# Kernel optimization log

Measured on AMD Instinct MI355X. Metric: run time of the kernel, lower is better.

Reference implementation:

```python
import jax, jax.numpy as jnp
import numpy as np

SH_DIM = 9                      # (sh_deg+1)^2, sh_deg=2
DATA_DIM = SH_DIM * 3 + 1       # 28
FINE = 8
COARSE = 32
RADIUS = 1.3
NUM_ATOMS = 16
BATCH = 128
STEP = (RADIUS * 2.0 / COARSE / FINE) / 2.0   # fine_voxel_len / 2
N_INTRS = COARSE * 3 * 2 * FINE               # 1536


def sh_encode(dirs):
    # degree-2 real spherical harmonics bases, [.., 9]
    x, y, z = dirs[..., 0], dirs[..., 1], dirs[..., 2]
    C0 = 0.28209479177387814
    C1 = 0.4886025119029199
    C2 = (1.0925484305920792, -1.0925484305920792, 0.31539156525252005,
          -1.0925484305920792, 0.5462742152960396)
    return jnp.stack([
        jnp.full_like(x, C0), -C1 * y, C1 * z, -C1 * x,
        C2[0] * x * y, C2[1] * y * z, C2[2] * (2.0 * z * z - x * x - y * y),
        C2[3] * x * z, C2[4] * (x * x - y * y)], axis=-1)


def dict_interp(grid, atoms, pts):
    # pts: [N,3] normalized to [0,1). grid: [COARSE^3, A]. atoms: [FINE^3, A, D].
    # coarse voxel -> dictionary coefficients; trilinear interp of atoms inside it.
    cpos = pts * COARSE
    cidx = jnp.clip(jnp.floor(cpos), 0, COARSE - 1)
    ci = cidx.astype(jnp.int32)
    coeff = grid[(ci[:, 0] * COARSE + ci[:, 1]) * COARSE + ci[:, 2]]  # [N, A]
    local = cpos - cidx                       # [0,1) within coarse voxel
    fpos = local * FINE - 0.5
    f0f = jnp.floor(fpos)
    w = fpos - f0f                            # trilinear weights
    f0 = f0f.astype(jnp.int32)
    out = jnp.zeros((pts.shape[0], DATA_DIM), dtype=pts.dtype)
    for dx in (0, 1):
        for dy in (0, 1):
            for dz in (0, 1):
                ix = jnp.clip(f0[:, 0] + dx, 0, FINE - 1)
                iy = jnp.clip(f0[:, 1] + dy, 0, FINE - 1)
                iz = jnp.clip(f0[:, 2] + dz, 0, FINE - 1)
                wt = ((w[:, 0] if dx else 1.0 - w[:, 0]) *
                      (w[:, 1] if dy else 1.0 - w[:, 1]) *
                      (w[:, 2] if dz else 1.0 - w[:, 2]))
                vals = jnp.einsum('na,nad->nd', coeff, atoms[(ix * FINE + iy) * FINE + iz])
                out = out + wt[:, None] * vals
    return out


def setup_inputs() -> dict:
    key = jax.random.key(0)
    k1, k2, k3, k4 = jax.random.split(key, 4)
    rays_o = jnp.array([0.0, 0.0, -2.0 * RADIUS]) + 0.05 * jax.random.normal(k1, (BATCH, 3), jnp.float32)
    d = 0.25 * jax.random.normal(k2, (BATCH, 3), jnp.float32) + jnp.array([0.0, 0.0, 1.0])
    rays_d = d / jnp.linalg.norm(d, axis=-1, keepdims=True)
    grid = 0.01 * jax.random.normal(k3, (COARSE ** 3, NUM_ATOMS), jnp.float32)
    atoms_sh = jax.random.uniform(k4, (FINE ** 3, NUM_ATOMS, DATA_DIM - 1), jnp.float32)
    atoms = jnp.concatenate([atoms_sh, jnp.full((FINE ** 3, NUM_ATOMS, 1), 0.01, jnp.float32)], -1)
    return {"rays_o": rays_o, "rays_d": rays_d, "grid": grid, "atoms": atoms, "grid_id": 0}


def reference(rays_o, rays_d, grid, atoms, grid_id):
    B = rays_o.shape[0]
    # ---- sample_proposal (no-grad in original) ----
    off_pos = (RADIUS - rays_o) / rays_d
    off_neg = (-RADIUS - rays_o) / rays_d
    start = jnp.max(jnp.minimum(off_pos, off_neg), axis=-1, keepdims=True)
    steps = jnp.arange(N_INTRS, dtype=rays_o.dtype)[None, :]
    intersections = jax.lax.stop_gradient(start + steps * STEP)        # [B, 1536]
    tsec = intersections[:, :-1]                                       # [B, M]
    M = N_INTRS - 1
    pts = rays_o[:, None, :] + tsec[:, :, None] * rays_d[:, None, :]   # [B, M, 3]
    mask = jnp.all((pts > -RADIUS) & (pts < RADIUS), axis=-1)          # [B, M]
    pts_n = jnp.clip((pts + RADIUS) / (2.0 * RADIUS), 0.0, 1.0 - 1e-6)
    pts_n = jax.lax.stop_gradient(pts_n).reshape(-1, 3)
    # ---- dictionary interpolation (computed densely, zeroed by mask) ----
    data = dict_interp(grid, atoms, pts_n).reshape(B, M, DATA_DIM)
    sigma = jax.nn.relu(jnp.where(mask, data[..., -1], 0.0))           # [B, M]
    # ---- sigma -> alpha / weights ----
    dists = (intersections[:, 1:] - intersections[:, :-1]) * jnp.linalg.norm(rays_d, axis=-1, keepdims=True)
    alpha = 1.0 - jnp.exp(-sigma * dists)
    trans = jnp.concatenate([jnp.ones((B, 1), alpha.dtype),
                             jnp.cumprod(1.0 - alpha + 1e-10, axis=-1)[:, :-1]], axis=-1)
    abs_light = alpha * trans                                          # [B, M]
    # ---- SH -> rgb, composite ----
    sh_mult = sh_encode(rays_d)[:, None, None, :]                      # [B,1,1,9]
    sh = data[..., :-1].reshape(B, M, 3, SH_DIM)
    rgb_raw = jnp.where(mask[..., None], jnp.sum(sh_mult * sh, axis=-1), 0.0)  # [B,M,3]
    rgb = jnp.sum(abs_light[..., None] * jax.nn.sigmoid(rgb_raw), axis=1)
    rgb = rgb + (1.0 - jnp.sum(abs_light, axis=-1))[:, None]           # white background
    depth = jnp.sum(abs_light * tsec, axis=-1)
    return rgb, alpha, depth
```

## Files before the change

kernel.cpp:

```cpp
#include <hip/hip_runtime.h>

typedef unsigned int u32;

#define MSAMP 1535
#define NS 1024
#define RADF 1.3f
#define STEPF ((float)(1.3 * 2.0 / 32.0 / 8.0 / 2.0))
#define NCELLG 32768
#define CSCALE 0.06f
#define PRANGE 4.0f

#if __has_builtin(__builtin_amdgcn_sdot4)
#define SDOT4(a, b, c) __builtin_amdgcn_sdot4((a), (b), (c), false)
#else
static __device__ __forceinline__ int SDOT4(int a, int b, int c) {
#pragma unroll
    for (int i = 0; i < 4; i++) {
        int ai = (a << (24 - 8 * i)) >> 24;
        int bi = (b << (24 - 8 * i)) >> 24;
        c += ai * bi;
    }
    return c;
}
#endif

__device__ __forceinline__ u32 q4(float a, float b, float c, float d, float S) {
    int i0 = (int)rintf(fminf(fmaxf(a * S, -127.0f), 127.0f));
    int i1 = (int)rintf(fminf(fmaxf(b * S, -127.0f), 127.0f));
    int i2 = (int)rintf(fminf(fmaxf(c * S, -127.0f), 127.0f));
    int i3 = (int)rintf(fminf(fmaxf(d * S, -127.0f), 127.0f));
    return (u32)(i0 & 255) | ((u32)(i1 & 255) << 8) | ((u32)(i2 & 255) << 16)
         | ((u32)(i3 & 255) << 24);
}

__global__ __launch_bounds__(256) void k_prep(const float* __restrict__ rd,
                                              const float* __restrict__ atoms,
                                              const float* __restrict__ grid,
                                              uint4* __restrict__ Pq,
                                              uint4* __restrict__ gridq) {
    __shared__ __align__(16) float af[448];
    int b = blockIdx.x, t = threadIdx.x;
    if (b < 512) {
        if (t < 112) ((float4*)af)[t] = ((const float4*)(atoms + b * 448))[t];
        int r = t & 127;
        float dx = rd[r * 3 + 0], dy = rd[r * 3 + 1], dz = rd[r * 3 + 2];
        float shm[9];
        shm[0] = 0.28209479177387814f;
        shm[1] = -0.4886025119029199f * dy;
        shm[2] =  0.4886025119029199f * dz;
        shm[3] = -0.4886025119029199f * dx;
        shm[4] =  1.0925484305920792f * dx * dy;
        shm[5] = -1.0925484305920792f * dy * dz;
        shm[6] =  0.31539156525252005f * (2.0f * dz * dz - dx * dx - dy * dy);
        shm[7] = -1.0925484305920792f * dx * dz;
        shm[8] =  0.5462742152960396f * (dx * dx - dy * dy);
        __syncthreads();
#pragma unroll
        for (int iter = 0; iter < 2; iter++) {
            int ch = (t >> 7) + 2 * iter;
            u32 w[4] = {0u, 0u, 0u, 0u};
            if (ch < 3) {
                const float S = 127.0f / PRANGE;
#pragma unroll
                for (int a = 0; a < 16; a++) {
                    const float* ap = af + a * 28 + ch * 9;
                    float p = shm[0] * ap[0];
#pragma unroll
                    for (int k = 1; k < 9; k++) p = fmaf(shm[k], ap[k], p);
                    int q = (int)rintf(fminf(fmaxf(p * S, -127.0f), 127.0f));
                    w[a >> 2] |= ((u32)(q & 255)) << (8 * (a & 3));
                }
            } else {
#pragma unroll
                for (int a = 0; a < 16; a++) {
                    float p = af[a * 28 + 27];
                    int q = (int)rintf(fminf(fmaxf(p * 127.0f, -127.0f), 127.0f));
                    w[a >> 2] |= ((u32)(q & 255)) << (8 * (a & 3));
                }
            }
            Pq[b * 512 + r * 4 + ch] = make_uint4(w[0], w[1], w[2], w[3]);
        }
    } else {
        int cell = (b - 512) * 256 + t;
        const float4* gp = (const float4*)(grid + cell * 16);
        float4 c0 = gp[0], c1 = gp[1], c2 = gp[2], c3 = gp[3];
        const float S = 127.0f / CSCALE;
        uint4 outv;
        outv.x = q4(c0.x, c0.y, c0.z, c0.w, S);
        outv.y = q4(c1.x, c1.y, c1.z, c1.w, S);
        outv.z = q4(c2.x, c2.y, c2.z, c2.w, S);
        outv.w = q4(c3.x, c3.y, c3.z, c3.w, S);
        gridq[cell] = outv;
    }
}

__global__ __launch_bounds__(1024) void k_main(const float* __restrict__ ro,
                                               const float* __restrict__ rd,
                                               const uint4* __restrict__ gridq,
                                               const uint4* __restrict__ Pq,
                                               float* __restrict__ rgb_out,
                                               float* __restrict__ alpha_out,
                                               float* __restrict__ depth_out) {
    __shared__ __align__(16) signed char hl[512 * 80];
    __shared__ float wprod[16];
    __shared__ float wred[16][5];
    int ray = blockIdx.x;
    int t = threadIdx.x;
    int lane = t & 63, wave = t >> 6;

#pragma unroll
    for (int i = 0; i < 2; i++) {
        int idx = i * 1024 + t;
        int cell = idx >> 2, part = idx & 3;
        uint4 v = Pq[cell * 512 + ray * 4 + part];
        *(uint4*)&hl[cell * 80 + part * 16] = v;
    }

    int abase = ray * MSAMP;
    if (NS + t < MSAMP) alpha_out[abase + NS + t] = 0.0f;

    float ox = ro[ray * 3 + 0], oy = ro[ray * 3 + 1], oz = ro[ray * 3 + 2];
    float dx = rd[ray * 3 + 0], dy = rd[ray * 3 + 1], dz = rd[ray * 3 + 2];
    float a0 = ( RADF - ox) / dx, b0 = (-RADF - ox) / dx;
    float a1 = ( RADF - oy) / dy, b1 = (-RADF - oy) / dy;
    float a2 = ( RADF - oz) / dz, b2 = (-RADF - oz) / dz;
    float st = fmaxf(fmaxf(fminf(a0, b0), fminf(a1, b1)), fminf(a2, b2));
    float nrm = sqrtf(dx * dx + dy * dy + dz * dz);

    __syncthreads();

    float tm = st + (float)t * STEPF;
    float px = ox + tm * dx, py = oy + tm * dy, pz = oz + tm * dz;
    bool inb = (px > -RADF) && (px < RADF) && (py > -RADF) && (py < RADF)
            && (pz > -RADF) && (pz < RADF);

    float acc[4] = {0.0f, 0.0f, 0.0f, 0.0f};
    if (inb) {
        const float inv2R = 1.0f / 2.6f;
        float pnx = fminf(fmaxf((px + RADF) * inv2R, 0.0f), 0.999999f);
        float pny = fminf(fmaxf((py + RADF) * inv2R, 0.0f), 0.999999f);
        float pnz = fminf(fmaxf((pz + RADF) * inv2R, 0.0f), 0.999999f);

        float cpx = pnx * 32.0f, cpy = pny * 32.0f, cpz = pnz * 32.0f;
        float cfx = floorf(cpx), cfy = floorf(cpy), cfz = floorf(cpz);
        int cix = (int)cfx, ciy = (int)cfy, ciz = (int)cfz;

        float fpx = (cpx - cfx) * 8.0f - 0.5f;
        float fpy = (cpy - cfy) * 8.0f - 0.5f;
        float fpz = (cpz - cfz) * 8.0f - 0.5f;
        float ffx = floorf(fpx), ffy = floorf(fpy), ffz = floorf(fpz);
        int f0x = (int)ffx, f0y = (int)ffy, f0z = (int)ffz;
        float wx = fpx - ffx, wy = fpy - ffy, wz = fpz - ffz;

        int ixa[2] = { max(f0x, 0), min(f0x + 1, 7) };
        int iya[2] = { max(f0y, 0), min(f0y + 1, 7) };
        int iza[2] = { max(f0z, 0), min(f0z + 1, 7) };
        float wxa[2] = { 1.0f - wx, wx };
        float wya[2] = { 1.0f - wy, wy };
        float wza[2] = { 1.0f - wz, wz };

        uint4 cq = gridq[(cix * 32 + ciy) * 32 + ciz];

#pragma unroll
        for (int cx = 0; cx < 2; cx++)
#pragma unroll
        for (int cy = 0; cy < 2; cy++)
#pragma unroll
        for (int cz = 0; cz < 2; cz++) {
            float wt = wxa[cx] * wya[cy] * wza[cz];
            int cb = ((ixa[cx] * 8 + iya[cy]) * 8 + iza[cz]) * 80;
#pragma unroll
            for (int j = 0; j < 4; j++) {
                uint4 qa = *(const uint4*)&hl[cb + j * 16];
                int di = SDOT4((int)qa.x, (int)cq.x, 0);
                di = SDOT4((int)qa.y, (int)cq.y, di);
                di = SDOT4((int)qa.z, (int)cq.z, di);
                di = SDOT4((int)qa.w, (int)cq.w, di);
                acc[j] = fmaf(wt, (float)di, acc[j]);
            }
        }
    }

    const float QSC = CSCALE / (127.0f * 127.0f);
    const float RSC = QSC * PRANGE;
    float sigma = fmaxf(acc[3] * QSC, 0.0f);
    float alpha = 1.0f - __expf(-sigma * STEPF * nrm);
    float r0 = 1.0f / (1.0f + __expf(-acc[0] * RSC));
    float r1 = 1.0f / (1.0f + __expf(-acc[1] * RSC));
    float r2 = 1.0f / (1.0f + __expf(-acc[2] * RSC));
    alpha_out[abase + t] = alpha;

    float p = 1.0f - alpha + 1e-10f;
    float incl = p;
#pragma unroll
    for (int off = 1; off < 64; off <<= 1) {
        float vv = __shfl_up(incl, off);
        if (lane >= off) incl *= vv;
    }
    if (lane == 63) wprod[wave] = incl;
    __syncthreads();
    float excl = __shfl_up(incl, 1);
    if (lane == 0) excl = 1.0f;
    for (int w = 0; w < 16; w++) if (w < wave) excl *= wprod[w];

    float w_ = alpha * excl;
    float vals[5] = { w_ * r0, w_ * r1, w_ * r2, w_ * tm, w_ };
#pragma unroll
    for (int i = 0; i < 5; i++) {
        float v = vals[i];
        v += __shfl_xor(v, 1);  v += __shfl_xor(v, 2);  v += __shfl_xor(v, 4);
        v += __shfl_xor(v, 8);  v += __shfl_xor(v, 16); v += __shfl_xor(v, 32);
        if (lane == 0) wred[wave][i] = v;
    }
    __syncthreads();
    if (t == 0) {
        float res[5];
#pragma unroll
        for (int i = 0; i < 5; i++) {
            float r_ = 0.0f;
            for (int w = 0; w < 16; w++) r_ += wred[w][i];
            res[i] = r_;
        }
        float omw = 1.0f - res[4];
        rgb_out[ray * 3 + 0] = res[0] + omw;
        rgb_out[ray * 3 + 1] = res[1] + omw;
        rgb_out[ray * 3 + 2] = res[2] + omw;
        depth_out[ray] = res[3];
    }
}

extern "C" void kernel_launch(void* const* d_in, const int* in_sizes, int n_in,
                              void* d_out, int out_size, void* d_ws, size_t ws_size,
                              hipStream_t stream) {
    const float* ro    = (const float*)d_in[0];
    const float* rd    = (const float*)d_in[1];
    const float* grid  = (const float*)d_in[2];
    const float* atoms = (const float*)d_in[3];
    int B = in_sizes[0] / 3;

    uint4* gridq = (uint4*)d_ws;
    uint4* Pq    = (uint4*)((char*)d_ws + 524288);

    float* out       = (float*)d_out;
    float* rgb_out   = out;
    float* alpha_out = out + B * 3;
    float* depth_out = out + B * 3 + B * MSAMP;

    hipLaunchKernelGGL(k_prep, dim3(640), dim3(256), 0, stream,
                       rd, atoms, grid, Pq, gridq);
    hipLaunchKernelGGL(k_main, dim3(B), dim3(1024), 0, stream,
                       ro, rd, (const uint4*)gridq, (const uint4*)Pq,
                       rgb_out, alpha_out, depth_out);
}
```

Before: 74.84 us.

## Shrink LDS atom stride to 72 bytes, transpose atoms in prep, issue global loads early

```diff
diff --git a/kernel.cpp b/kernel.cpp
--- a/kernel.cpp
+++ b/kernel.cpp
@@ -9,6 +9,7 @@
 #define NCELLG 32768
 #define CSCALE 0.06f
 #define PRANGE 4.0f
+#define HSTRIDE 72
 
 #if __has_builtin(__builtin_amdgcn_sdot4)
 #define SDOT4(a, b, c) __builtin_amdgcn_sdot4((a), (b), (c), false)
@@ -38,10 +39,19 @@
                                               const float* __restrict__ grid,
                                               uint4* __restrict__ Pq,
                                               uint4* __restrict__ gridq) {
-    __shared__ __align__(16) float af[448];
+    __shared__ __align__(16) float af2[28 * 16];
     int b = blockIdx.x, t = threadIdx.x;
     if (b < 512) {
-        if (t < 112) ((float4*)af)[t] = ((const float4*)(atoms + b * 448))[t];
+        if (t < 112) {
+            float4 v = ((const float4*)(atoms + b * 448))[t];
+            int i0 = t * 4;
+#pragma unroll
+            for (int u = 0; u < 4; u++) {
+                int i = i0 + u;
+                int a = i / 28, d = i - a * 28;
+                af2[d * 16 + a] = (&v.x)[u];
+            }
+        }
         int r = t & 127;
         float dx = rd[r * 3 + 0], dy = rd[r * 3 + 1], dz = rd[r * 3 + 2];
         float shm[9];
@@ -58,25 +68,45 @@
 #pragma unroll
         for (int iter = 0; iter < 2; iter++) {
             int ch = (t >> 7) + 2 * iter;
-            u32 w[4] = {0u, 0u, 0u, 0u};
+            float p[16];
+            float S;
             if (ch < 3) {
-                const float S = 127.0f / PRANGE;
-#pragma unroll
-                for (int a = 0; a < 16; a++) {
-                    const float* ap = af + a * 28 + ch * 9;
-                    float p = shm[0] * ap[0];
-#pragma unroll
-                    for (int k = 1; k < 9; k++) p = fmaf(shm[k], ap[k], p);
-                    int q = (int)rintf(fminf(fmaxf(p * S, -127.0f), 127.0f));
-                    w[a >> 2] |= ((u32)(q & 255)) << (8 * (a & 3));
+                S = 127.0f / PRANGE;
+#pragma unroll
+                for (int k = 0; k < 9; k++) {
+                    const float4* row = (const float4*)&af2[(ch * 9 + k) * 16];
+                    float4 q0 = row[0], q1 = row[1], q2 = row[2], q3 = row[3];
+                    float s = shm[k];
+                    if (k == 0) {
+                        p[0]=s*q0.x;  p[1]=s*q0.y;  p[2]=s*q0.z;  p[3]=s*q0.w;
+                        p[4]=s*q1.x;  p[5]=s*q1.y;  p[6]=s*q1.z;  p[7]=s*q1.w;
+                        p[8]=s*q2.x;  p[9]=s*q2.y;  p[10]=s*q2.z; p[11]=s*q2.w;
+                        p[12]=s*q3.x; p[13]=s*q3.y; p[14]=s*q3.z; p[15]=s*q3.w;
+                    } else {
+                        p[0]=fmaf(s,q0.x,p[0]);   p[1]=fmaf(s,q0.y,p[1]);
+                        p[2]=fmaf(s,q0.z,p[2]);   p[3]=fmaf(s,q0.w,p[3]);
+                        p[4]=fmaf(s,q1.x,p[4]);   p[5]=fmaf(s,q1.y,p[5]);
+                        p[6]=fmaf(s,q1.z,p[6]);   p[7]=fmaf(s,q1.w,p[7]);
+                        p[8]=fmaf(s,q2.x,p[8]);   p[9]=fmaf(s,q2.y,p[9]);
+                        p[10]=fmaf(s,q2.z,p[10]); p[11]=fmaf(s,q2.w,p[11]);
+                        p[12]=fmaf(s,q3.x,p[12]); p[13]=fmaf(s,q3.y,p[13]);
+                        p[14]=fmaf(s,q3.z,p[14]); p[15]=fmaf(s,q3.w,p[15]);
+                    }
                 }
             } else {
-#pragma unroll
-                for (int a = 0; a < 16; a++) {
-                    float p = af[a * 28 + 27];
-                    int q = (int)rintf(fminf(fmaxf(p * 127.0f, -127.0f), 127.0f));
-                    w[a >> 2] |= ((u32)(q & 255)) << (8 * (a & 3));
-                }
+                S = 127.0f;
+                const float4* row = (const float4*)&af2[27 * 16];
+                float4 q0 = row[0], q1 = row[1], q2 = row[2], q3 = row[3];
+                p[0]=q0.x;  p[1]=q0.y;  p[2]=q0.z;  p[3]=q0.w;
+                p[4]=q1.x;  p[5]=q1.y;  p[6]=q1.z;  p[7]=q1.w;
+                p[8]=q2.x;  p[9]=q2.y;  p[10]=q2.z; p[11]=q2.w;
+                p[12]=q3.x; p[13]=q3.y; p[14]=q3.z; p[15]=q3.w;
+            }
+            u32 w[4] = {0u, 0u, 0u, 0u};
+#pragma unroll
+            for (int a = 0; a < 16; a++) {
+                int q = (int)rintf(fminf(fmaxf(p[a] * S, -127.0f), 127.0f));
+                w[a >> 2] |= ((u32)(q & 255)) << (8 * (a & 3));
             }
             Pq[b * 512 + r * 4 + ch] = make_uint4(w[0], w[1], w[2], w[3]);
         }
@@ -101,20 +131,17 @@
                                                float* __restrict__ rgb_out,
                                                float* __restrict__ alpha_out,
                                                float* __restrict__ depth_out) {
-    __shared__ __align__(16) signed char hl[512 * 80];
+    __shared__ __align__(16) signed char hl[512 * HSTRIDE];
     __shared__ float wprod[16];
     __shared__ float wred[16][5];
     int ray = blockIdx.x;
     int t = threadIdx.x;
     int lane = t & 63, wave = t >> 6;
 
-#pragma unroll
-    for (int i = 0; i < 2; i++) {
-        int idx = i * 1024 + t;
-        int cell = idx >> 2, part = idx & 3;
-        uint4 v = Pq[cell * 512 + ray * 4 + part];
-        *(uint4*)&hl[cell * 80 + part * 16] = v;
-    }
+    int cell0 = t >> 2,           part0 = t & 3;
+    int cell1 = (1024 + t) >> 2,  part1 = t & 3;
+    uint4 v0 = Pq[cell0 * 512 + ray * 4 + part0];
+    uint4 v1 = Pq[cell1 * 512 + ray * 4 + part1];
 
     int abase = ray * MSAMP;
     if (NS + t < MSAMP) alpha_out[abase + NS + t] = 0.0f;
@@ -127,6 +154,14 @@
     float st = fmaxf(fmaxf(fminf(a0, b0), fminf(a1, b1)), fminf(a2, b2));
     float nrm = sqrtf(dx * dx + dy * dy + dz * dz);
 
+    {
+        int ba0 = cell0 * HSTRIDE + part0 * 16;
+        int ba1 = cell1 * HSTRIDE + part1 * 16;
+        *(uint2*)&hl[ba0]     = make_uint2(v0.x, v0.y);
+        *(uint2*)&hl[ba0 + 8] = make_uint2(v0.z, v0.w);
+        *(uint2*)&hl[ba1]     = make_uint2(v1.x, v1.y);
+        *(uint2*)&hl[ba1 + 8] = make_uint2(v1.z, v1.w);
+    }
     __syncthreads();
 
     float tm = st + (float)t * STEPF;
@@ -168,14 +203,15 @@
 #pragma unroll
         for (int cz = 0; cz < 2; cz++) {
             float wt = wxa[cx] * wya[cy] * wza[cz];
-            int cb = ((ixa[cx] * 8 + iya[cy]) * 8 + iza[cz]) * 80;
+            int cb = ((ixa[cx] * 8 + iya[cy]) * 8 + iza[cz]) * HSTRIDE;
 #pragma unroll
             for (int j = 0; j < 4; j++) {
-                uint4 qa = *(const uint4*)&hl[cb + j * 16];
+                uint2 qa = *(const uint2*)&hl[cb + j * 16];
+                uint2 qb = *(const uint2*)&hl[cb + j * 16 + 8];
                 int di = SDOT4((int)qa.x, (int)cq.x, 0);
                 di = SDOT4((int)qa.y, (int)cq.y, di);
-                di = SDOT4((int)qa.z, (int)cq.z, di);
-                di = SDOT4((int)qa.w, (int)cq.w, di);
+                di = SDOT4((int)qb.x, (int)cq.z, di);
+                di = SDOT4((int)qb.y, (int)cq.w, di);
                 acc[j] = fmaf(wt, (float)di, acc[j]);
             }
         }
```

After: 73.53 us. About the same (-1.8%).
